# Optimization experiments

Hardware: AMD Instinct MI355X
Metric: run time of the kernel (lower is better)

## Reference

```python
import jax, jax.numpy as jnp
import numpy as np

IN = 1    # input feature dim (hardcoded in NN)
H = 10    # LSTM hidden size (hardcoded in NN)
B = 8192  # batch
T = 256   # sequence length


def setup_inputs() -> dict:
    key = jax.random.key(0)
    ks = jax.random.split(key, 12)
    s = 0.1  # init scale for mus (mimics blitz posterior_mu_init spread)
    RHO0 = -3.0  # posterior_rho_init from the module
    return {
        "x": jax.random.normal(ks[0], (B, T, IN), jnp.float32),
        # BayesianLSTM variational parameters (blitz layout: (in, 4*H), (H, 4*H), (4*H,))
        "w_ih_mu": jax.random.normal(ks[1], (IN, 4 * H), jnp.float32) * s,
        "w_ih_rho": jnp.full((IN, 4 * H), RHO0, jnp.float32),
        "w_hh_mu": jax.random.normal(ks[2], (H, 4 * H), jnp.float32) * s,
        "w_hh_rho": jnp.full((H, 4 * H), RHO0, jnp.float32),
        "b_mu": jax.random.normal(ks[3], (4 * H,), jnp.float32) * s,
        "b_rho": jnp.full((4 * H,), RHO0, jnp.float32),
        # reparameterization noise, sampled once per forward call in blitz
        "eps_ih": jax.random.normal(ks[4], (IN, 4 * H), jnp.float32),
        "eps_hh": jax.random.normal(ks[5], (H, 4 * H), jnp.float32),
        "eps_b": jax.random.normal(ks[6], (4 * H,), jnp.float32),
        # deterministic linear head nn.Linear(10, 1)
        "lin_w": jax.random.normal(ks[7], (1, H), jnp.float32) * s,
        "lin_b": jnp.zeros((1,), jnp.float32),
    }


def reference(x, w_ih_mu, w_ih_rho, w_hh_mu, w_hh_rho, b_mu, b_rho,
              eps_ih, eps_hh, eps_b, lin_w, lin_b):
    sp = jax.nn.softplus
    # sample weights: w = mu + log1p(exp(rho)) * eps
    w_ih = w_ih_mu + sp(w_ih_rho) * eps_ih   # (IN, 4H)
    w_hh = w_hh_mu + sp(w_hh_rho) * eps_hh   # (H, 4H)
    b = b_mu + sp(b_rho) * eps_b             # (4H,)

    # precompute input contribution for all timesteps: (B, T, 4H)
    x_proj = jnp.einsum('bti,ig->btg', x, w_ih) + b

    def step(carry, xg):
        h, c = carry                      # (B, H) each
        gates = xg + h @ w_hh             # (B, 4H)
        i = jax.nn.sigmoid(gates[:, :H])
        f = jax.nn.sigmoid(gates[:, H:2 * H])
        g = jnp.tanh(gates[:, 2 * H:3 * H])
        o = jax.nn.sigmoid(gates[:, 3 * H:])
        c = f * c + i * g
        h = o * jnp.tanh(c)
        return (h, c), None

    h0 = jnp.zeros((x.shape[0], H), x.dtype)
    (h_last, _), _ = jax.lax.scan(step, (h0, h0), jnp.swapaxes(x_proj, 0, 1))
    # NN takes hidden_seq[:, -1, :] == final hidden state, then linear head
    return h_last @ lin_w.T + lin_b  # (B, 1)
```

## Files before the change

### kernel.cpp

```cpp
#include <hip/hip_runtime.h>
#include <math.h>

#define T_LEN 256
#define HID 10

typedef float v2f __attribute__((ext_vector_type(2)));

__device__ __forceinline__ v2f mk2(float a, float b) { v2f r; r.x = a; r.y = b; return r; }
__device__ __forceinline__ v2f splat2(float a) { return mk2(a, a); }

__device__ __forceinline__ float softplus_f(float x) {
    return fmaxf(x, 0.0f) + log1pf(expf(-fabsf(x)));
}
__device__ __forceinline__ float samp(const float* mu, const float* rho,
                                      const float* eps, int i) {
    return mu[i] + softplus_f(rho[i]) * eps[i];
}

__device__ __forceinline__ float fast_sigmoid(float x) {
    float e = __builtin_amdgcn_exp2f(-1.442695040888963f * x);
    return __builtin_amdgcn_rcpf(1.0f + e);
}
__device__ __forceinline__ float fast_tanh(float x) {
    float e = __builtin_amdgcn_exp2f(2.885390081777927f * x);
    return fmaf(-2.0f, __builtin_amdgcn_rcpf(e + 1.0f), 1.0f);
}

struct Wreg {
    v2f whh01[HID], whh23[HID];
    v2f wih01, wih23, b01, b23;
};

__device__ __forceinline__ float lstm_step(const Wreg& w, float xt,
                                           float4 h0, float4 h1, float4 h2,
                                           float& c)
{
    v2f x2 = splat2(xt);
    v2f e01 = __builtin_elementwise_fma(x2, w.wih01, w.b01);
    v2f e23 = __builtin_elementwise_fma(x2, w.wih23, w.b23);
    v2f o01 = w.whh01[1] * splat2(h0.y);
    v2f o23 = w.whh23[1] * splat2(h0.y);
    e01 = __builtin_elementwise_fma(splat2(h0.x), w.whh01[0], e01);
    e23 = __builtin_elementwise_fma(splat2(h0.x), w.whh23[0], e23);
    o01 = __builtin_elementwise_fma(splat2(h0.w), w.whh01[3], o01);
    o23 = __builtin_elementwise_fma(splat2(h0.w), w.whh23[3], o23);
    e01 = __builtin_elementwise_fma(splat2(h0.z), w.whh01[2], e01);
    e23 = __builtin_elementwise_fma(splat2(h0.z), w.whh23[2], e23);
    o01 = __builtin_elementwise_fma(splat2(h1.y), w.whh01[5], o01);
    o23 = __builtin_elementwise_fma(splat2(h1.y), w.whh23[5], o23);
    e01 = __builtin_elementwise_fma(splat2(h1.x), w.whh01[4], e01);
    e23 = __builtin_elementwise_fma(splat2(h1.x), w.whh23[4], e23);
    o01 = __builtin_elementwise_fma(splat2(h1.w), w.whh01[7], o01);
    o23 = __builtin_elementwise_fma(splat2(h1.w), w.whh23[7], o23);
    e01 = __builtin_elementwise_fma(splat2(h1.z), w.whh01[6], e01);
    e23 = __builtin_elementwise_fma(splat2(h1.z), w.whh23[6], e23);
    o01 = __builtin_elementwise_fma(splat2(h2.y), w.whh01[9], o01);
    o23 = __builtin_elementwise_fma(splat2(h2.y), w.whh23[9], o23);
    e01 = __builtin_elementwise_fma(splat2(h2.x), w.whh01[8], e01);
    e23 = __builtin_elementwise_fma(splat2(h2.x), w.whh23[8], e23);
    v2f a01 = e01 + o01;
    v2f a23 = e23 + o23;
    float ig = fast_sigmoid(a01.x);
    float fg = fast_sigmoid(a01.y);
    float gg = fast_tanh(a23.x);
    float og = fast_sigmoid(a23.y);
    c = fmaf(fg, c, ig * gg);
    return og * fast_tanh(c);
}

__global__ __launch_bounds__(64) void bayes_lstm_kernel(
    const float* __restrict__ x,
    const float* __restrict__ w_ih_mu, const float* __restrict__ w_ih_rho,
    const float* __restrict__ w_hh_mu, const float* __restrict__ w_hh_rho,
    const float* __restrict__ b_mu,    const float* __restrict__ b_rho,
    const float* __restrict__ eps_ih,  const float* __restrict__ eps_hh,
    const float* __restrict__ eps_b,
    const float* __restrict__ lin_w,   const float* __restrict__ lin_b,
    float* __restrict__ out, int n_elem)
{
    __shared__ __align__(16) float hbuf[7 * 20];

    const int lane  = threadIdx.x;
    const int g     = lane / 10;
    const int k     = lane - g * 10;
    const int gbase = g * 10;
    const int b     = blockIdx.x * 6 + g;
    const bool valid = (g < 6) && (b < n_elem);
    const int b_eff = (b < n_elem) ? b : (n_elem - 1);
    float* hb = hbuf + g * 20;

    Wreg w;
    const int c0 = k, c1 = HID + k, c2 = 2 * HID + k, c3 = 3 * HID + k;
    w.wih01 = mk2(samp(w_ih_mu, w_ih_rho, eps_ih, c0), samp(w_ih_mu, w_ih_rho, eps_ih, c1));
    w.wih23 = mk2(samp(w_ih_mu, w_ih_rho, eps_ih, c2), samp(w_ih_mu, w_ih_rho, eps_ih, c3));
    w.b01   = mk2(samp(b_mu, b_rho, eps_b, c0), samp(b_mu, b_rho, eps_b, c1));
    w.b23   = mk2(samp(b_mu, b_rho, eps_b, c2), samp(b_mu, b_rho, eps_b, c3));
#pragma unroll
    for (int j = 0; j < HID; ++j) {
        w.whh01[j] = mk2(samp(w_hh_mu, w_hh_rho, eps_hh, j * 4 * HID + c0),
                         samp(w_hh_mu, w_hh_rho, eps_hh, j * 4 * HID + c1));
        w.whh23[j] = mk2(samp(w_hh_mu, w_hh_rho, eps_hh, j * 4 * HID + c2),
                         samp(w_hh_mu, w_hh_rho, eps_hh, j * 4 * HID + c3));
    }
    const float lw = lin_w[k];

    hb[k] = 0.f;
    if (k < 2) hb[10 + k] = 0.f;

    float c = 0.f, hk = 0.f;
    const float* xr = x + (size_t)b_eff * T_LEN;
    const bool ldx = (k < 8);
    float xc = ldx ? xr[k] : 0.f;
    const float4* p = (const float4*)hb;

    for (int ch = 0; ch < 32; ++ch) {
        float xn = 0.f;
        if (ldx && ch < 31) xn = xr[(ch + 1) * 8 + k];
#pragma unroll
        for (int ti = 0; ti < 8; ++ti) {
            float4 h0 = p[0], h1 = p[1], h2 = p[2];
            float xt = __shfl(xc, gbase + ti, 64);
            hk = lstm_step(w, xt, h0, h1, h2, c);
            hb[k] = hk;
        }
        xc = xn;
    }

    hb[k] = hk * lw;
    if (k == 0 && valid) {
        float4 s0 = p[0], s1 = p[1], s2 = p[2];
        out[b] = (s0.x + s0.y + s0.z + s0.w)
               + (s1.x + s1.y + s1.z + s1.w)
               + (s2.x + s2.y + s2.z + s2.w) + lin_b[0];
    }
}

extern "C" void kernel_launch(void* const* d_in, const int* in_sizes, int n_in,
                              void* d_out, int out_size, void* d_ws, size_t ws_size,
                              hipStream_t stream) {
    const float* x        = (const float*)d_in[0];
    const float* w_ih_mu  = (const float*)d_in[1];
    const float* w_ih_rho = (const float*)d_in[2];
    const float* w_hh_mu  = (const float*)d_in[3];
    const float* w_hh_rho = (const float*)d_in[4];
    const float* b_mu     = (const float*)d_in[5];
    const float* b_rho    = (const float*)d_in[6];
    const float* eps_ih   = (const float*)d_in[7];
    const float* eps_hh   = (const float*)d_in[8];
    const float* eps_b    = (const float*)d_in[9];
    const float* lin_w    = (const float*)d_in[10];
    const float* lin_b    = (const float*)d_in[11];
    float* out = (float*)d_out;

    const int n_b = in_sizes[0] / T_LEN;
    dim3 grid((n_b + 5) / 6), block(64);
    hipLaunchKernelGGL(bayes_lstm_kernel, grid, block, 0, stream,
                       x, w_ih_mu, w_ih_rho, w_hh_mu, w_hh_rho, b_mu, b_rho,
                       eps_ih, eps_hh, eps_b, lin_w, lin_b, out, n_b);
}
```

Measured before the change: 165.4 us.

## Exchange hidden state via ds_bpermute instead of LDS, pack 4 sequences per wave

```diff
diff --git a/kernel.cpp b/kernel.cpp
--- a/kernel.cpp
+++ b/kernel.cpp
@@ -26,38 +26,41 @@
     return fmaf(-2.0f, __builtin_amdgcn_rcpf(e + 1.0f), 1.0f);
 }
 
+__device__ __forceinline__ float bperm_f(int addr, float v) {
+    return __int_as_float(__builtin_amdgcn_ds_bpermute(addr, __float_as_int(v)));
+}
+
 struct Wreg {
     v2f whh01[HID], whh23[HID];
     v2f wih01, wih23, b01, b23;
 };
 
 __device__ __forceinline__ float lstm_step(const Wreg& w, float xt,
-                                           float4 h0, float4 h1, float4 h2,
-                                           float& c)
+                                           const float h[HID], float& c)
 {
     v2f x2 = splat2(xt);
     v2f e01 = __builtin_elementwise_fma(x2, w.wih01, w.b01);
     v2f e23 = __builtin_elementwise_fma(x2, w.wih23, w.b23);
-    v2f o01 = w.whh01[1] * splat2(h0.y);
-    v2f o23 = w.whh23[1] * splat2(h0.y);
-    e01 = __builtin_elementwise_fma(splat2(h0.x), w.whh01[0], e01);
-    e23 = __builtin_elementwise_fma(splat2(h0.x), w.whh23[0], e23);
-    o01 = __builtin_elementwise_fma(splat2(h0.w), w.whh01[3], o01);
-    o23 = __builtin_elementwise_fma(splat2(h0.w), w.whh23[3], o23);
-    e01 = __builtin_elementwise_fma(splat2(h0.z), w.whh01[2], e01);
-    e23 = __builtin_elementwise_fma(splat2(h0.z), w.whh23[2], e23);
-    o01 = __builtin_elementwise_fma(splat2(h1.y), w.whh01[5], o01);
-    o23 = __builtin_elementwise_fma(splat2(h1.y), w.whh23[5], o23);
-    e01 = __builtin_elementwise_fma(splat2(h1.x), w.whh01[4], e01);
-    e23 = __builtin_elementwise_fma(splat2(h1.x), w.whh23[4], e23);
-    o01 = __builtin_elementwise_fma(splat2(h1.w), w.whh01[7], o01);
-    o23 = __builtin_elementwise_fma(splat2(h1.w), w.whh23[7], o23);
-    e01 = __builtin_elementwise_fma(splat2(h1.z), w.whh01[6], e01);
-    e23 = __builtin_elementwise_fma(splat2(h1.z), w.whh23[6], e23);
-    o01 = __builtin_elementwise_fma(splat2(h2.y), w.whh01[9], o01);
-    o23 = __builtin_elementwise_fma(splat2(h2.y), w.whh23[9], o23);
-    e01 = __builtin_elementwise_fma(splat2(h2.x), w.whh01[8], e01);
-    e23 = __builtin_elementwise_fma(splat2(h2.x), w.whh23[8], e23);
+    v2f o01 = w.whh01[1] * splat2(h[1]);
+    v2f o23 = w.whh23[1] * splat2(h[1]);
+    e01 = __builtin_elementwise_fma(splat2(h[0]), w.whh01[0], e01);
+    e23 = __builtin_elementwise_fma(splat2(h[0]), w.whh23[0], e23);
+    o01 = __builtin_elementwise_fma(splat2(h[3]), w.whh01[3], o01);
+    o23 = __builtin_elementwise_fma(splat2(h[3]), w.whh23[3], o23);
+    e01 = __builtin_elementwise_fma(splat2(h[2]), w.whh01[2], e01);
+    e23 = __builtin_elementwise_fma(splat2(h[2]), w.whh23[2], e23);
+    o01 = __builtin_elementwise_fma(splat2(h[5]), w.whh01[5], o01);
+    o23 = __builtin_elementwise_fma(splat2(h[5]), w.whh23[5], o23);
+    e01 = __builtin_elementwise_fma(splat2(h[4]), w.whh01[4], e01);
+    e23 = __builtin_elementwise_fma(splat2(h[4]), w.whh23[4], e23);
+    o01 = __builtin_elementwise_fma(splat2(h[7]), w.whh01[7], o01);
+    o23 = __builtin_elementwise_fma(splat2(h[7]), w.whh23[7], o23);
+    e01 = __builtin_elementwise_fma(splat2(h[6]), w.whh01[6], e01);
+    e23 = __builtin_elementwise_fma(splat2(h[6]), w.whh23[6], e23);
+    o01 = __builtin_elementwise_fma(splat2(h[9]), w.whh01[9], o01);
+    o23 = __builtin_elementwise_fma(splat2(h[9]), w.whh23[9], o23);
+    e01 = __builtin_elementwise_fma(splat2(h[8]), w.whh01[8], e01);
+    e23 = __builtin_elementwise_fma(splat2(h[8]), w.whh23[8], e23);
     v2f a01 = e01 + o01;
     v2f a23 = e23 + o23;
     float ig = fast_sigmoid(a01.x);
@@ -78,16 +81,13 @@
     const float* __restrict__ lin_w,   const float* __restrict__ lin_b,
     float* __restrict__ out, int n_elem)
 {
-    __shared__ __align__(16) float hbuf[7 * 20];
-
     const int lane  = threadIdx.x;
     const int g     = lane / 10;
     const int k     = lane - g * 10;
-    const int gbase = g * 10;
-    const int b     = blockIdx.x * 6 + g;
-    const bool valid = (g < 6) && (b < n_elem);
-    const int b_eff = (b < n_elem) ? b : (n_elem - 1);
-    float* hb = hbuf + g * 20;
+    const bool valid = (g < 4);
+    const int gbase = valid ? g * 10 : 0;
+    const int b     = blockIdx.x * 4 + g;
+    const int b_eff = (valid && b < n_elem) ? b : 0;
 
     Wreg w;
     const int c0 = k, c1 = HID + k, c2 = 2 * HID + k, c3 = 3 * HID + k;
@@ -102,36 +102,43 @@
         w.whh23[j] = mk2(samp(w_hh_mu, w_hh_rho, eps_hh, j * 4 * HID + c2),
                          samp(w_hh_mu, w_hh_rho, eps_hh, j * 4 * HID + c3));
     }
-    const float lw = lin_w[k];
 
-    hb[k] = 0.f;
-    if (k < 2) hb[10 + k] = 0.f;
+    int ha[HID];
+#pragma unroll
+    for (int j = 0; j < HID; ++j) ha[j] = (gbase + j) * 4;
+    int xa[8];
+#pragma unroll
+    for (int t = 0; t < 8; ++t) xa[t] = (gbase + t) * 4;
 
     float c = 0.f, hk = 0.f;
     const float* xr = x + (size_t)b_eff * T_LEN;
     const bool ldx = (k < 8);
     float xc = ldx ? xr[k] : 0.f;
-    const float4* p = (const float4*)hb;
 
     for (int ch = 0; ch < 32; ++ch) {
         float xn = 0.f;
         if (ldx && ch < 31) xn = xr[(ch + 1) * 8 + k];
+        float xt[8];
+#pragma unroll
+        for (int t = 0; t < 8; ++t) xt[t] = bperm_f(xa[t], xc);
 #pragma unroll
         for (int ti = 0; ti < 8; ++ti) {
-            float4 h0 = p[0], h1 = p[1], h2 = p[2];
-            float xt = __shfl(xc, gbase + ti, 64);
-            hk = lstm_step(w, xt, h0, h1, h2, c);
-            hb[k] = hk;
+            float h[HID];
+#pragma unroll
+            for (int j = 0; j < HID; ++j) h[j] = bperm_f(ha[j], hk);
+            hk = lstm_step(w, xt[ti], h, c);
         }
         xc = xn;
     }
 
-    hb[k] = hk * lw;
-    if (k == 0 && valid) {
-        float4 s0 = p[0], s1 = p[1], s2 = p[2];
-        out[b] = (s0.x + s0.y + s0.z + s0.w)
-               + (s1.x + s1.y + s1.z + s1.w)
-               + (s2.x + s2.y + s2.z + s2.w) + lin_b[0];
+    float hf[HID];
+#pragma unroll
+    for (int j = 0; j < HID; ++j) hf[j] = bperm_f(ha[j], hk);
+    if (k == 0 && valid && b < n_elem) {
+        float acc = lin_b[0];
+#pragma unroll
+        for (int j = 0; j < HID; ++j) acc = fmaf(lin_w[j], hf[j], acc);
+        out[b] = acc;
     }
 }
 
@@ -153,7 +160,7 @@
     float* out = (float*)d_out;
 
     const int n_b = in_sizes[0] / T_LEN;
-    dim3 grid((n_b + 5) / 6), block(64);
+    dim3 grid((n_b + 3) / 4), block(64);
     hipLaunchKernelGGL(bayes_lstm_kernel, grid, block, 0, stream,
                        x, w_ih_mu, w_ih_rho, w_hh_mu, w_hh_rho, b_mu, b_rho,
                        eps_ih, eps_hh, eps_b, lin_w, lin_b, out, n_b);
```

Result: no change. 167.8 us (+1.5%).

## Exchange LSTM hidden state via DPP row rotation instead of LDS

Applied to the files above, without the earlier changes.

```diff
diff --git a/kernel.cpp b/kernel.cpp
--- a/kernel.cpp
+++ b/kernel.cpp
@@ -26,38 +26,44 @@
     return fmaf(-2.0f, __builtin_amdgcn_rcpf(e + 1.0f), 1.0f);
 }
 
+#define ROTF(hi, R) __int_as_float(__builtin_amdgcn_mov_dpp((hi), 0x120 + (R), 0xF, 0xF, true))
+
 struct Wreg {
-    v2f whh01[HID], whh23[HID];
+    v2f wsel01[16], wsel23[16];
     v2f wih01, wih23, b01, b23;
 };
 
-__device__ __forceinline__ float lstm_step(const Wreg& w, float xt,
-                                           float4 h0, float4 h1, float4 h2,
+__device__ __forceinline__ float lstm_step(const Wreg& w, float xt, float hk,
                                            float& c)
 {
+    const int hi = __float_as_int(hk);
     v2f x2 = splat2(xt);
     v2f e01 = __builtin_elementwise_fma(x2, w.wih01, w.b01);
     v2f e23 = __builtin_elementwise_fma(x2, w.wih23, w.b23);
-    v2f o01 = w.whh01[1] * splat2(h0.y);
-    v2f o23 = w.whh23[1] * splat2(h0.y);
-    e01 = __builtin_elementwise_fma(splat2(h0.x), w.whh01[0], e01);
-    e23 = __builtin_elementwise_fma(splat2(h0.x), w.whh23[0], e23);
-    o01 = __builtin_elementwise_fma(splat2(h0.w), w.whh01[3], o01);
-    o23 = __builtin_elementwise_fma(splat2(h0.w), w.whh23[3], o23);
-    e01 = __builtin_elementwise_fma(splat2(h0.z), w.whh01[2], e01);
-    e23 = __builtin_elementwise_fma(splat2(h0.z), w.whh23[2], e23);
-    o01 = __builtin_elementwise_fma(splat2(h1.y), w.whh01[5], o01);
-    o23 = __builtin_elementwise_fma(splat2(h1.y), w.whh23[5], o23);
-    e01 = __builtin_elementwise_fma(splat2(h1.x), w.whh01[4], e01);
-    e23 = __builtin_elementwise_fma(splat2(h1.x), w.whh23[4], e23);
-    o01 = __builtin_elementwise_fma(splat2(h1.w), w.whh01[7], o01);
-    o23 = __builtin_elementwise_fma(splat2(h1.w), w.whh23[7], o23);
-    e01 = __builtin_elementwise_fma(splat2(h1.z), w.whh01[6], e01);
-    e23 = __builtin_elementwise_fma(splat2(h1.z), w.whh23[6], e23);
-    o01 = __builtin_elementwise_fma(splat2(h2.y), w.whh01[9], o01);
-    o23 = __builtin_elementwise_fma(splat2(h2.y), w.whh23[9], o23);
-    e01 = __builtin_elementwise_fma(splat2(h2.x), w.whh01[8], e01);
-    e23 = __builtin_elementwise_fma(splat2(h2.x), w.whh23[8], e23);
+    v2f o01 = w.wsel01[0] * splat2(hk);
+    v2f o23 = w.wsel23[0] * splat2(hk);
+#define RSTEP(R, A01, A23)                                            \
+    {                                                                 \
+        v2f hr = splat2(ROTF(hi, R));                                 \
+        A01 = __builtin_elementwise_fma(hr, w.wsel01[R], A01);        \
+        A23 = __builtin_elementwise_fma(hr, w.wsel23[R], A23);        \
+    }
+    RSTEP(1,  e01, e23)
+    RSTEP(2,  o01, o23)
+    RSTEP(3,  e01, e23)
+    RSTEP(4,  o01, o23)
+    RSTEP(5,  e01, e23)
+    RSTEP(6,  o01, o23)
+    RSTEP(7,  e01, e23)
+    RSTEP(8,  o01, o23)
+    RSTEP(9,  e01, e23)
+    RSTEP(10, o01, o23)
+    RSTEP(11, e01, e23)
+    RSTEP(12, o01, o23)
+    RSTEP(13, e01, e23)
+    RSTEP(14, o01, o23)
+    RSTEP(15, e01, e23)
+#undef RSTEP
     v2f a01 = e01 + o01;
     v2f a23 = e23 + o23;
     float ig = fast_sigmoid(a01.x);
@@ -78,61 +84,58 @@
     const float* __restrict__ lin_w,   const float* __restrict__ lin_b,
     float* __restrict__ out, int n_elem)
 {
-    __shared__ __align__(16) float hbuf[7 * 20];
-
-    const int lane  = threadIdx.x;
-    const int g     = lane / 10;
-    const int k     = lane - g * 10;
-    const int gbase = g * 10;
-    const int b     = blockIdx.x * 6 + g;
-    const bool valid = (g < 6) && (b < n_elem);
+    const int lane = threadIdx.x & 63;
+    const int k    = lane & 15;
+    const int g    = lane >> 4;
+    const int b    = blockIdx.x * 4 + g;
     const int b_eff = (b < n_elem) ? b : (n_elem - 1);
-    float* hb = hbuf + g * 20;
+    const bool un  = (k < HID);
 
     Wreg w;
-    const int c0 = k, c1 = HID + k, c2 = 2 * HID + k, c3 = 3 * HID + k;
-    w.wih01 = mk2(samp(w_ih_mu, w_ih_rho, eps_ih, c0), samp(w_ih_mu, w_ih_rho, eps_ih, c1));
-    w.wih23 = mk2(samp(w_ih_mu, w_ih_rho, eps_ih, c2), samp(w_ih_mu, w_ih_rho, eps_ih, c3));
-    w.b01   = mk2(samp(b_mu, b_rho, eps_b, c0), samp(b_mu, b_rho, eps_b, c1));
-    w.b23   = mk2(samp(b_mu, b_rho, eps_b, c2), samp(b_mu, b_rho, eps_b, c3));
+    w.wih01 = splat2(0.f); w.wih23 = splat2(0.f);
+    w.b01 = splat2(0.f);   w.b23 = splat2(0.f);
+    if (un) {
+        const int c0 = k, c1 = HID + k, c2 = 2 * HID + k, c3 = 3 * HID + k;
+        w.wih01 = mk2(samp(w_ih_mu, w_ih_rho, eps_ih, c0), samp(w_ih_mu, w_ih_rho, eps_ih, c1));
+        w.wih23 = mk2(samp(w_ih_mu, w_ih_rho, eps_ih, c2), samp(w_ih_mu, w_ih_rho, eps_ih, c3));
+        w.b01   = mk2(samp(b_mu, b_rho, eps_b, c0), samp(b_mu, b_rho, eps_b, c1));
+        w.b23   = mk2(samp(b_mu, b_rho, eps_b, c2), samp(b_mu, b_rho, eps_b, c3));
+    }
 #pragma unroll
-    for (int j = 0; j < HID; ++j) {
-        w.whh01[j] = mk2(samp(w_hh_mu, w_hh_rho, eps_hh, j * 4 * HID + c0),
-                         samp(w_hh_mu, w_hh_rho, eps_hh, j * 4 * HID + c1));
-        w.whh23[j] = mk2(samp(w_hh_mu, w_hh_rho, eps_hh, j * 4 * HID + c2),
-                         samp(w_hh_mu, w_hh_rho, eps_hh, j * 4 * HID + c3));
+    for (int r = 0; r < 16; ++r) {
+        const int idx = (k - r) & 15;
+        if (un && idx < HID) {
+            const int base = idx * 4 * HID;
+            w.wsel01[r] = mk2(samp(w_hh_mu, w_hh_rho, eps_hh, base + k),
+                              samp(w_hh_mu, w_hh_rho, eps_hh, base + HID + k));
+            w.wsel23[r] = mk2(samp(w_hh_mu, w_hh_rho, eps_hh, base + 2 * HID + k),
+                              samp(w_hh_mu, w_hh_rho, eps_hh, base + 3 * HID + k));
+        } else {
+            w.wsel01[r] = splat2(0.f);
+            w.wsel23[r] = splat2(0.f);
+        }
     }
-    const float lw = lin_w[k];
-
-    hb[k] = 0.f;
-    if (k < 2) hb[10 + k] = 0.f;
 
     float c = 0.f, hk = 0.f;
-    const float* xr = x + (size_t)b_eff * T_LEN;
-    const bool ldx = (k < 8);
-    float xc = ldx ? xr[k] : 0.f;
-    const float4* p = (const float4*)hb;
-
-    for (int ch = 0; ch < 32; ++ch) {
-        float xn = 0.f;
-        if (ldx && ch < 31) xn = xr[(ch + 1) * 8 + k];
-#pragma unroll
-        for (int ti = 0; ti < 8; ++ti) {
-            float4 h0 = p[0], h1 = p[1], h2 = p[2];
-            float xt = __shfl(xc, gbase + ti, 64);
-            hk = lstm_step(w, xt, h0, h1, h2, c);
-            hb[k] = hk;
-        }
-        xc = xn;
+    const float4* xv = (const float4*)(x + (size_t)b_eff * T_LEN);
+    float4 xq = xv[0];
+    for (int ch = 0; ch < 64; ++ch) {
+        const int nx = (ch < 63) ? ch + 1 : 63;
+        float4 xn = xv[nx];
+        hk = lstm_step(w, xq.x, hk, c);
+        hk = lstm_step(w, xq.y, hk, c);
+        hk = lstm_step(w, xq.z, hk, c);
+        hk = lstm_step(w, xq.w, hk, c);
+        xq = xn;
     }
 
-    hb[k] = hk * lw;
-    if (k == 0 && valid) {
-        float4 s0 = p[0], s1 = p[1], s2 = p[2];
-        out[b] = (s0.x + s0.y + s0.z + s0.w)
-               + (s1.x + s1.y + s1.z + s1.w)
-               + (s2.x + s2.y + s2.z + s2.w) + lin_b[0];
-    }
+    const float lw = un ? lin_w[k] : 0.f;
+    float pa = hk * lw;
+    pa += __shfl_xor(pa, 1, 16);
+    pa += __shfl_xor(pa, 2, 16);
+    pa += __shfl_xor(pa, 4, 16);
+    pa += __shfl_xor(pa, 8, 16);
+    if (k == 0 && b < n_elem) out[b] = pa + lin_b[0];
 }
 
 extern "C" void kernel_launch(void* const* d_in, const int* in_sizes, int n_in,
@@ -153,7 +156,7 @@
     float* out = (float*)d_out;
 
     const int n_b = in_sizes[0] / T_LEN;
-    dim3 grid((n_b + 5) / 6), block(64);
+    dim3 grid((n_b + 3) / 4), block(64);
     hipLaunchKernelGGL(bayes_lstm_kernel, grid, block, 0, stream,
                        x, w_ih_mu, w_ih_rho, w_hh_mu, w_hh_rho, b_mu, b_rho,
                        eps_ih, eps_hh, eps_b, lin_w, lin_b, out, n_b);
```

After: 188.1 us. 1.14x slower.
